# Optimization experiments

Hardware: AMD Instinct MI355X
Metric: run time of the kernel (lower is better)

## Reference

```python
import jax, jax.numpy as jnp
import numpy as np

EMBED_DIM = 1024
N_HEADS = 16
HEAD_DIM = EMBED_DIM // N_HEADS
B, N = 4, 2048


def setup_inputs() -> dict:
    key = jax.random.key(0)
    k1, k2, k3, k4, k5 = jax.random.split(key, 5)
    x = jax.random.normal(k1, (B, N, EMBED_DIM), dtype=jnp.float32)
    # Per-head kqv Linear weights stacked: torch Linear(embed_dim, 3*head_dim)
    # torch stores weight as [out, in]; we store transposed [in, out] per head.
    scale = 1.0 / np.sqrt(EMBED_DIM)
    W_kqv = jax.random.uniform(k2, (N_HEADS, EMBED_DIM, 3 * HEAD_DIM), dtype=jnp.float32, minval=-scale, maxval=scale)
    b_kqv = jax.random.uniform(k3, (N_HEADS, 3 * HEAD_DIM), dtype=jnp.float32, minval=-scale, maxval=scale)
    W_proj = jax.random.uniform(k4, (EMBED_DIM, EMBED_DIM), dtype=jnp.float32, minval=-scale, maxval=scale)
    b_proj = jax.random.uniform(k5, (EMBED_DIM,), dtype=jnp.float32, minval=-scale, maxval=scale)
    return {"x": x, "W_kqv": W_kqv, "b_kqv": b_kqv, "W_proj": W_proj, "b_proj": b_proj}


def reference(x, W_kqv, b_kqv, W_proj, b_proj):
    Bx, Nx, D = x.shape
    H = W_kqv.shape[0]
    hd = W_kqv.shape[2] // 3
    # All per-head kqv projections at once: [B, H, N, 3*hd]
    kqv = jnp.einsum('bnd,hde->bhne', x, W_kqv) + b_kqv[None, :, None, :]
    # chunk order in source is (k, q, v)
    k, q, v = jnp.split(kqv, 3, axis=-1)
    # scores scaled by sqrt(head_dim) (D1 in attention_scores is head dim)
    scores = jnp.einsum('bhqd,bhkd->bhqk', q, k) / jnp.sqrt(jnp.float32(hd))
    causal = jnp.tril(jnp.ones((Nx, Nx), dtype=bool))  # [N, N]
    scores = jnp.where(causal[None, None, :, :], scores, -jnp.inf)
    attn = jax.nn.softmax(scores, axis=-1)
    sa = jnp.einsum('bhqk,bhkd->bhqd', attn, v)  # [B, H, N, hd]
    # concat heads along feature dim (head order preserved)
    sa = sa.transpose(0, 2, 1, 3).reshape(Bx, Nx, H * hd)
    # output projection: torch Linear with weight [out, in] -> y = sa @ W^T + b;
    # here W_proj is stored as [in, out]
    return sa @ W_proj + b_proj
```

## Files before the change

### kernel.cpp

```cpp
#include <hip/hip_runtime.h>
#include <math.h>

#define EMBED   1024
#define NHEADS  16
#define HD      64
#define BATCH   4
#define SEQ     2048
#define MROWS   (BATCH*SEQ)
#define NKV     8388608ull

typedef short short8 __attribute__((ext_vector_type(8)));
typedef float floatx4 __attribute__((ext_vector_type(4)));

__device__ __forceinline__ unsigned short f2b(float f) {
    union { float f; unsigned u; } v; v.f = f;
    unsigned r = v.u + 0x7FFFu + ((v.u >> 16) & 1u);
    return (unsigned short)(r >> 16);
}
__device__ __forceinline__ unsigned short f2b_fast(float f) {
    union { float f; unsigned u; } v; v.f = f;
    return (unsigned short)((v.u + 0x8000u) >> 16);
}

#define GLDS16(gp, lp) __builtin_amdgcn_global_load_lds( \
    (const __attribute__((address_space(1))) unsigned int*)(gp), \
    (__attribute__((address_space(3))) unsigned int*)(lp), 16, 0, 0)

__global__ __launch_bounds__(256) void convert_x(
    const float* __restrict__ x, unsigned short* __restrict__ x16)
{
    size_t idx = ((size_t)blockIdx.x * 256 + threadIdx.x) * 8;
    float4 a = *(const float4*)(x + idx);
    float4 b = *(const float4*)(x + idx + 4);
    ushort4 u0, u1;
    u0.x = f2b(a.x); u0.y = f2b(a.y); u0.z = f2b(a.z); u0.w = f2b(a.w);
    u1.x = f2b(b.x); u1.y = f2b(b.y); u1.z = f2b(b.z); u1.w = f2b(b.w);
    *(ushort4*)(x16 + idx) = u0;
    *(ushort4*)(x16 + idx + 4) = u1;
}

__global__ __launch_bounds__(256) void prep_wkqv(
    const float* __restrict__ Wk, unsigned short* __restrict__ Wt)
{
    __shared__ float tile[32][33];
    const int h = blockIdx.z;
    const int k0 = blockIdx.x * 32, e0 = blockIdx.y * 32;
    const float* inh = Wk + (size_t)h * 1024 * 192;
    const int tx = threadIdx.x & 31, ty = threadIdx.x >> 5;
    #pragma unroll
    for (int i = 0; i < 4; i++)
        tile[ty + i * 8][tx] = inh[(size_t)(k0 + ty + i * 8) * 192 + e0 + tx];
    __syncthreads();
    #pragma unroll
    for (int i = 0; i < 4; i++) {
        int e = e0 + ty + i * 8;
        int cp = (e >> 6) * 1024 + h * 64 + (e & 63);
        Wt[(size_t)cp * 1024 + k0 + tx] = f2b(tile[tx][ty + i * 8]);
    }
}

__global__ __launch_bounds__(256) void transpose_w(
    const float* __restrict__ in, unsigned short* __restrict__ outp, int R, int C)
{
    __shared__ float tile[32][33];
    const int r0 = blockIdx.x * 32, c0 = blockIdx.y * 32;
    const int tx = threadIdx.x & 31, ty = threadIdx.x >> 5;
    #pragma unroll
    for (int i = 0; i < 4; i++)
        tile[ty + i * 8][tx] = in[(size_t)(r0 + ty + i * 8) * C + c0 + tx];
    __syncthreads();
    #pragma unroll
    for (int i = 0; i < 4; i++)
        outp[(size_t)(c0 + ty + i * 8) * R + r0 + tx] = f2b(tile[tx][ty + i * 8]);
}

__device__ __forceinline__ void mainloop_128x256(
    const unsigned short* __restrict__ Ag,
    const unsigned short* __restrict__ Bg,
    unsigned short* smem,
    int row0, int col0, floatx4 (&acc)[4][4])
{
    const int t = threadIdx.x;
    const int wave = t >> 6, lane = t & 63;
    const int lr = lane & 15, quad = lane >> 4;
    const int wr = wave >> 2, wc = wave & 3;
    const int swz8 = ((lane & 7) ^ ((lane >> 3) & 7)) * 8;
    const int c0 = (quad ^ (lr & 7)) * 8;
    const int c1 = ((4 + quad) ^ (lr & 7)) * 8;

    #pragma unroll
    for (int m = 0; m < 4; m++)
        #pragma unroll
        for (int n = 0; n < 4; n++) acc[m][n] = (floatx4){0.f, 0.f, 0.f, 0.f};

#define STG(G, R0, KC, L) do { \
    _Pragma("unroll") \
    for (int i_ = 0; i_ < 2; i_++) { \
        int rl_ = i_ * 64 + wave * 8 + (lane >> 3); \
        GLDS16((G) + (size_t)((R0) + rl_) * 1024 + (KC) + swz8, \
               (L) + rl_ * 64 + (lane & 7) * 8); \
    } } while (0)

    STG(Ag, row0,       0,  smem);
    STG(Bg, col0,       0,  smem + 8192);
    STG(Bg, col0 + 128, 0,  smem + 16384);
    STG(Bg, col0,       64, smem + 24576 + 8192);
    STG(Bg, col0 + 128, 64, smem + 24576 + 16384);
    asm volatile("s_waitcnt vmcnt(4)" ::: "memory");
    __builtin_amdgcn_s_barrier();

    #pragma unroll 2
    for (int j = 0; j < 16; ++j) {
        unsigned short* Ab = smem + (j & 1) * 24576;
        unsigned short* Bb = Ab + 8192;
        unsigned short* An = smem + ((j + 1) & 1) * 24576;
        const unsigned short* pA = Ab + (wr * 64 + lr) * 64;
        const unsigned short* pB = Bb + (wc * 64 + lr) * 64;

        short8 af0[4], af1[4], b0[4], b1[4];

        #pragma unroll
        for (int m = 0; m < 4; m++) af0[m] = *(const short8*)(pA + m * 1024 + c0);
        #pragma unroll
        for (int n = 0; n < 4; n++) b0[n] = *(const short8*)(pB + n * 1024 + c0);
        #pragma unroll
        for (int n = 0; n < 4; n++) b1[n] = *(const short8*)(pB + n * 1024 + c1);
        if (j < 15) STG(Ag, row0, (j + 1) * 64, An);
        __builtin_amdgcn_s_barrier();
        asm volatile("s_waitcnt lgkmcnt(0)" ::: "memory");
        __builtin_amdgcn_s_setprio(1);
        #pragma unroll
        for (int m = 0; m < 4; m++)
            #pragma unroll
            for (int n = 0; n < 4; n++)
                acc[m][n] = __builtin_amdgcn_mfma_f32_16x16x32_bf16(af0[m], b0[n], acc[m][n], 0, 0, 0);
        __builtin_amdgcn_s_setprio(0);
        __builtin_amdgcn_s_barrier();

        #pragma unroll
        for (int m = 0; m < 4; m++) af1[m] = *(const short8*)(pA + m * 1024 + c1);
        if (j < 14) {
            STG(Bg, col0,       (j + 2) * 64, Bb);
            STG(Bg, col0 + 128, (j + 2) * 64, Bb + 8192);
        }
        __builtin_amdgcn_s_barrier();
        asm volatile("s_waitcnt lgkmcnt(0)" ::: "memory");
        __builtin_amdgcn_s_setprio(1);
        #pragma unroll
        for (int m = 0; m < 4; m++)
            #pragma unroll
            for (int n = 0; n < 4; n++)
                acc[m][n] = __builtin_amdgcn_mfma_f32_16x16x32_bf16(af1[m], b1[n], acc[m][n], 0, 0, 0);
        __builtin_amdgcn_s_setprio(0);
        if (j < 14)       asm volatile("s_waitcnt vmcnt(4)" ::: "memory");
        else if (j == 14) asm volatile("s_waitcnt vmcnt(0)" ::: "memory");
        __builtin_amdgcn_s_barrier();
    }
#undef STG
}

__global__ __launch_bounds__(512, 2) void gemm_kqv(
    const unsigned short* __restrict__ A,
    const unsigned short* __restrict__ Bt,
    const float* __restrict__ bk,
    unsigned short* __restrict__ Kb16,
    unsigned short* __restrict__ Qb16,
    unsigned short* __restrict__ Vt16)
{
    __shared__ unsigned short smem[49152];

    const int mt = blockIdx.x;
    const int ct = blockIdx.y;
    const int row0 = mt * 128, col0 = ct * 256;

    floatx4 acc[4][4];
    mainloop_128x256(A, Bt, smem, row0, col0, acc);

    const int t = threadIdx.x;
    const int wave = t >> 6, lane = t & 63;
    const int lr = lane & 15, quad = lane >> 4;
    const int wr = wave >> 2, wc = wave & 3;

    unsigned short* W = smem + wave * 4096;
    const int sec = ct >> 2;
    const int h = ((ct & 3) << 2) + wc;
    const int bidx = row0 >> 11;
    const int rbase = (row0 & 2047) + wr * 64;

    float bias[4];
    #pragma unroll
    for (int n = 0; n < 4; n++) bias[n] = bk[h * 192 + sec * 64 + n * 16 + lr];

    if (sec < 2) {
        const float scl = (sec == 1) ? (0.125f * 1.44269504089f) : 1.0f;
        #pragma unroll
        for (int m = 0; m < 4; m++)
            #pragma unroll
            for (int n = 0; n < 4; n++) {
                int es = (n * 16 + lr) ^ (quad << 4);
                #pragma unroll
                for (int r = 0; r < 4; r++)
                    W[(m * 16 + quad * 4 + r) * 64 + es] = f2b((acc[m][n][r] + bias[n]) * scl);
            }
        __syncthreads();
        unsigned short* dst = ((sec == 0) ? Kb16 : Qb16)
                              + ((size_t)(bidx * 16 + h) * 2048 + rbase) * 64;
        const int rrow = lane >> 3, chunk = lane & 7;
        #pragma unroll
        for (int p = 0; p < 8; p++) {
            int row = p * 8 + rrow;
            int ch = chunk ^ (((row >> 2) & 3) << 1);
            *(float4*)(dst + (size_t)row * 64 + chunk * 8) =
                *(const float4*)(W + row * 64 + ch * 8);
        }
    } else {
        #pragma unroll
        for (int m = 0; m < 4; m++)
            #pragma unroll
            for (int n = 0; n < 4; n++) {
                int e = n * 16 + lr;
                ushort4 pk;
                pk.x = f2b(acc[m][n][0] + bias[n]);
                pk.y = f2b(acc[m][n][1] + bias[n]);
                pk.z = f2b(acc[m][n][2] + bias[n]);
                pk.w = f2b(acc[m][n][3] + bias[n]);
                int mp = m ^ (lr & 3);
                *(ushort4*)(W + e * 64 + mp * 16 + quad * 4) = pk;
            }
        __syncthreads();
        unsigned short* dstV = Vt16 + (size_t)(bidx * 16 + h) * 64 * 2048 + rbase;
        const int ev = lane >> 3, chunkR = lane & 7;
        #pragma unroll
        for (int p = 0; p < 8; p++) {
            int e = p * 8 + ev;
            int ch = chunkR ^ ((e & 3) << 1);
            *(float4*)(dstV + (size_t)e * 2048 + chunkR * 8) =
                *(const float4*)(W + e * 64 + ch * 8);
        }
    }
}

__global__ __launch_bounds__(256, 2) void attn_mfma(
    const unsigned short* __restrict__ Kb,
    const unsigned short* __restrict__ Qb,
    const unsigned short* __restrict__ Vt,
    unsigned short* __restrict__ sa)
{
    const int bx = blockIdx.x;
    const int bh = blockIdx.y;
    const int b = bh >> 4, h = bh & 15;
    const int wave = threadIdx.x >> 6;
    const int lane = threadIdx.x & 63;
    const int lr = lane & 15, quad = lane >> 4;
    const int qt_[2] = {bx, 15 - bx};

    __shared__ unsigned short Ks[64 * 64];
    __shared__ unsigned short Vs[64 * 64];
    __shared__ unsigned short Ps[4][2][16 * 72];

    const unsigned short* Kbh = Kb + (size_t)bh * 2048 * 64;
    const unsigned short* Vbh = Vt + (size_t)bh * 64 * 2048;
    const unsigned short* Qbh = Qb + (size_t)bh * 2048 * 64;

    short8 qf[2][2][2];
    #pragma unroll
    for (int tt = 0; tt < 2; tt++)
        #pragma unroll
        for (int s = 0; s < 2; s++) {
            const unsigned short* qp = Qbh +
                (size_t)(qt_[tt] * 128 + wave * 32 + s * 16 + lr) * 64 + quad * 8;
            qf[tt][s][0] = *(const short8*)(qp);
            qf[tt][s][1] = *(const short8*)(qp + 32);
        }

    floatx4 O[2][2][4];
    float ls[2][2][4];
    #pragma unroll
    for (int tt = 0; tt < 2; tt++)
        #pragma unroll
        for (int s = 0; s < 2; s++) {
            #pragma unroll
            for (int d = 0; d < 4; d++) O[tt][s][d] = (floatx4){0.f, 0.f, 0.f, 0.f};
            #pragma unroll
            for (int r = 0; r < 4; r++) ls[tt][s][r] = 0.f;
        }

    const int r_local = lane >> 3, cc = lane & 7;
    const int swz = cc ^ r_local;
    const int whalf = wave >> 1;

    const int ktmax = 2 * qt_[1] + 1;
    for (int kt = 0; kt <= ktmax; kt++) {
        const int k0 = kt * 64;
        __syncthreads();
        #pragma unroll
        for (int j = 0; j < 2; j++) {
            int R = wave * 16 + j * 8 + r_local;
            GLDS16(Kbh + (size_t)(k0 + R) * 64 + swz * 8, Ks + (wave * 16 + j * 8) * 64 + lane * 8);
            GLDS16(Vbh + (size_t)R * 2048 + k0 + swz * 8, Vs + (wave * 16 + j * 8) * 64 + lane * 8);
        }
        __syncthreads();

        #pragma unroll
        for (int tt = 0; tt < 2; tt++) {
            const int qt2 = qt_[tt];
            const int lim = 2 * qt2 + whalf;
            if (kt > lim) continue;

            floatx4 S[2][4];
            #pragma unroll
            for (int s = 0; s < 2; s++)
                #pragma unroll
                for (int a = 0; a < 4; a++) S[s][a] = (floatx4){0.f, 0.f, 0.f, 0.f};
            #pragma unroll
            for (int c = 0; c < 2; c++)
                #pragma unroll
                for (int a = 0; a < 4; a++) {
                    int R = a * 16 + lr;
                    short8 kf = *(const short8*)(Ks + R * 64 + (((c * 4 + quad) ^ (lr & 7)) * 8));
                    #pragma unroll
                    for (int s = 0; s < 2; s++)
                        S[s][a] = __builtin_amdgcn_mfma_f32_16x16x32_bf16(qf[tt][s][c], kf, S[s][a], 0, 0, 0);
                }

            if (kt == lim) {
                #pragma unroll
                for (int s = 0; s < 2; s++)
                    #pragma unroll
                    for (int a = 0; a < 4; a++) {
                        int col = k0 + a * 16 + lr;
                        #pragma unroll
                        for (int r = 0; r < 4; r++) {
                            int grow = qt2 * 128 + wave * 32 + s * 16 + quad * 4 + r;
                            if (col > grow) S[s][a][r] = -INFINITY;
                        }
                    }
            }

            #pragma unroll
            for (int s = 0; s < 2; s++)
                #pragma unroll
                for (int a = 0; a < 4; a++)
                    #pragma unroll
                    for (int r = 0; r < 4; r++) {
                        float p = __builtin_amdgcn_exp2f(S[s][a][r]);
                        ls[tt][s][r] += p;
                        Ps[wave][s][(quad * 4 + r) * 72 + a * 16 + lr] = f2b_fast(p);
                    }

            short8 pa[2][2];
            #pragma unroll
            for (int s = 0; s < 2; s++)
                #pragma unroll
                for (int c = 0; c < 2; c++)
                    pa[s][c] = *(const short8*)(Ps[wave][s] + lr * 72 + c * 32 + quad * 8);

            #pragma unroll
            for (int c = 0; c < 2; c++)
                #pragma unroll
                for (int d = 0; d < 4; d++) {
                    int R = d * 16 + lr;
                    short8 vf = *(const short8*)(Vs + R * 64 + (((c * 4 + quad) ^ (lr & 7)) * 8));
                    #pragma unroll
                    for (int s = 0; s < 2; s++)
                        O[tt][s][d] = __builtin_amdgcn_mfma_f32_16x16x32_bf16(pa[s][c], vf, O[tt][s][d], 0, 0, 0);
                }
        }
    }

    #pragma unroll
    for (int tt = 0; tt < 2; tt++)
        #pragma unroll
        for (int s = 0; s < 2; s++)
            #pragma unroll
            for (int r = 0; r < 4; r++) {
                float sm = ls[tt][s][r];
                sm += __shfl_xor(sm, 1);
                sm += __shfl_xor(sm, 2);
                sm += __shfl_xor(sm, 4);
                sm += __shfl_xor(sm, 8);
                float inv = 1.0f / sm;
                size_t base = ((size_t)(b * 2048 + qt_[tt] * 128 + wave * 32 + s * 16 + quad * 4 + r)) * 1024
                              + h * 64 + lr;
                #pragma unroll
                for (int d = 0; d < 4; d++)
                    sa[base + d * 16] = f2b(O[tt][s][d][r] * inv);
            }
}

__global__ __launch_bounds__(512, 2) void gemm_proj(
    const unsigned short* __restrict__ A,
    const unsigned short* __restrict__ Bt,
    const float* __restrict__ bp,
    float* __restrict__ out)
{
    __shared__ unsigned short smem[49152];

    const int mt = blockIdx.x;
    const int ct = blockIdx.y;
    const int row0 = mt * 128, col0 = ct * 256;

    floatx4 acc[4][4];
    mainloop_128x256(A, Bt, smem, row0, col0, acc);

    const int t = threadIdx.x;
    const int lane = t & 63, wave = t >> 6;
    const int lr = lane & 15, quad = lane >> 4;
    const int wr = wave >> 2, wc = wave & 3;

    float bias[4]; int cols[4];
    #pragma unroll
    for (int n = 0; n < 4; n++) {
        cols[n] = col0 + wc * 64 + n * 16 + lr;
        bias[n] = bp[cols[n]];
    }
    #pragma unroll
    for (int a = 0; a < 4; a++) {
        #pragma unroll
        for (int n = 0; n < 4; n++) {
            #pragma unroll
            for (int r = 0; r < 4; r++) {
                int m = row0 + wr * 64 + a * 16 + quad * 4 + r;
                out[(size_t)m * 1024 + cols[n]] = acc[a][n][r] + bias[n];
            }
        }
    }
}

extern "C" void kernel_launch(void* const* d_in, const int* in_sizes, int n_in,
                              void* d_out, int out_size, void* d_ws, size_t ws_size,
                              hipStream_t stream) {
    const float* x  = (const float*)d_in[0];
    const float* Wk = (const float*)d_in[1];
    const float* bk = (const float*)d_in[2];
    const float* Wp = (const float*)d_in[3];
    const float* bp = (const float*)d_in[4];
    float* out = (float*)d_out;

    unsigned short* Kb16 = (unsigned short*)d_ws;
    unsigned short* Qb16 = Kb16 + NKV;
    unsigned short* Vt16 = Qb16 + NKV;
    unsigned short* sa16 = Vt16 + NKV;
    unsigned short* x16  = sa16 + 8388608ull;
    unsigned short* Wt   = x16  + 8388608ull;
    unsigned short* Wpt  = Wt   + 3145728ull;

    convert_x<<<4096, 256, 0, stream>>>(x, x16);
    prep_wkqv<<<dim3(32, 6, 16), 256, 0, stream>>>(Wk, Wt);
    transpose_w<<<dim3(32, 32, 1), 256, 0, stream>>>(Wp, Wpt, 1024, 1024);
    gemm_kqv<<<dim3(64, 12), 512, 0, stream>>>(x16, Wt, bk, Kb16, Qb16, Vt16);
    attn_mfma<<<dim3(8, 64), 256, 0, stream>>>(Kb16, Qb16, Vt16, sa16);
    gemm_proj<<<dim3(64, 4), 512, 0, stream>>>(sa16, Wpt, bp, out);
}
```

Measured before the change: 245.4 us.

## Double-buffer K/V tiles in attention and swap grid dimension order

The attention kernel now keeps two LDS buffers for K and V. It issues the global-to-LDS loads for the next key tile before computing on the current one, and waits on vmcnt plus a barrier at the end of each iteration, replacing the two syncthreads per tile. The grid is also transposed so blockIdx.x walks batch-heads, which changes block scheduling order and L2 locality. The cost is doubled K/V LDS usage, which may affect occupancy at two blocks per CU.

Measured after the change: 234.3 us. 4.5% less time.

```diff
diff --git a/kernel.cpp b/kernel.cpp
--- a/kernel.cpp
+++ b/kernel.cpp
@@ -246,16 +246,16 @@
     const unsigned short* __restrict__ Vt,
     unsigned short* __restrict__ sa)
 {
-    const int bx = blockIdx.x;
-    const int bh = blockIdx.y;
+    const int bh = blockIdx.x;
+    const int bx = blockIdx.y;
     const int b = bh >> 4, h = bh & 15;
     const int wave = threadIdx.x >> 6;
     const int lane = threadIdx.x & 63;
     const int lr = lane & 15, quad = lane >> 4;
     const int qt_[2] = {bx, 15 - bx};
 
-    __shared__ unsigned short Ks[64 * 64];
-    __shared__ unsigned short Vs[64 * 64];
+    __shared__ unsigned short Ks[2][64 * 64];
+    __shared__ unsigned short Vs[2][64 * 64];
     __shared__ unsigned short Ps[4][2][16 * 72];
 
     const unsigned short* Kbh = Kb + (size_t)bh * 2048 * 64;
@@ -289,17 +289,33 @@
     const int swz = cc ^ r_local;
     const int whalf = wave >> 1;
 
+#define STAGE_KV(KT, BSEL) do { \
+    const int k0_ = (KT) * 64; \
+    _Pragma("unroll") \
+    for (int j_ = 0; j_ < 2; j_++) { \
+        int R_ = wave * 16 + j_ * 8 + r_local; \
+        GLDS16(Kbh + (size_t)(k0_ + R_) * 64 + swz * 8, \
+               &Ks[BSEL][0] + (wave * 16 + j_ * 8) * 64 + lane * 8); \
+        GLDS16(Vbh + (size_t)R_ * 2048 + k0_ + swz * 8, \
+               &Vs[BSEL][0] + (wave * 16 + j_ * 8) * 64 + lane * 8); \
+    } } while (0)
+
     const int ktmax = 2 * qt_[1] + 1;
+
+    STAGE_KV(0, 0);
+    asm volatile("s_waitcnt vmcnt(0)" ::: "memory");
+    __builtin_amdgcn_s_barrier();
+
     for (int kt = 0; kt <= ktmax; kt++) {
+        const int buf = kt & 1;
+        const unsigned short* Ksb = &Ks[buf][0];
+        const unsigned short* Vsb = &Vs[buf][0];
         const int k0 = kt * 64;
-        __syncthreads();
-        #pragma unroll
-        for (int j = 0; j < 2; j++) {
-            int R = wave * 16 + j * 8 + r_local;
-            GLDS16(Kbh + (size_t)(k0 + R) * 64 + swz * 8, Ks + (wave * 16 + j * 8) * 64 + lane * 8);
-            GLDS16(Vbh + (size_t)R * 2048 + k0 + swz * 8, Vs + (wave * 16 + j * 8) * 64 + lane * 8);
-        }
-        __syncthreads();
+
+        if (kt < ktmax) {
+            if (buf) STAGE_KV(kt + 1, 0);
+            else     STAGE_KV(kt + 1, 1);
+        }
 
         #pragma unroll
         for (int tt = 0; tt < 2; tt++) {
@@ -317,7 +333,7 @@
                 #pragma unroll
                 for (int a = 0; a < 4; a++) {
                     int R = a * 16 + lr;
-                    short8 kf = *(const short8*)(Ks + R * 64 + (((c * 4 + quad) ^ (lr & 7)) * 8));
+                    short8 kf = *(const short8*)(Ksb + R * 64 + (((c * 4 + quad) ^ (lr & 7)) * 8));
                     #pragma unroll
                     for (int s = 0; s < 2; s++)
                         S[s][a] = __builtin_amdgcn_mfma_f32_16x16x32_bf16(qf[tt][s][c], kf, S[s][a], 0, 0, 0);
@@ -360,13 +376,17 @@
                 #pragma unroll
                 for (int d = 0; d < 4; d++) {
                     int R = d * 16 + lr;
-                    short8 vf = *(const short8*)(Vs + R * 64 + (((c * 4 + quad) ^ (lr & 7)) * 8));
+                    short8 vf = *(const short8*)(Vsb + R * 64 + (((c * 4 + quad) ^ (lr & 7)) * 8));
                     #pragma unroll
                     for (int s = 0; s < 2; s++)
                         O[tt][s][d] = __builtin_amdgcn_mfma_f32_16x16x32_bf16(pa[s][c], vf, O[tt][s][d], 0, 0, 0);
                 }
         }
-    }
+
+        asm volatile("s_waitcnt vmcnt(0)" ::: "memory");
+        __builtin_amdgcn_s_barrier();
+    }
+#undef STAGE_KV
 
     #pragma unroll
     for (int tt = 0; tt < 2; tt++)
@@ -449,6 +469,6 @@
     prep_wkqv<<<dim3(32, 6, 16), 256, 0, stream>>>(Wk, Wt);
     transpose_w<<<dim3(32, 32, 1), 256, 0, stream>>>(Wp, Wpt, 1024, 1024);
     gemm_kqv<<<dim3(64, 12), 512, 0, stream>>>(x16, Wt, bk, Kb16, Qb16, Vt16);
-    attn_mfma<<<dim3(8, 64), 256, 0, stream>>>(Kb16, Qb16, Vt16, sa16);
+    attn_mfma<<<dim3(64, 8), 256, 0, stream>>>(Kb16, Qb16, Vt16, sa16);
     gemm_proj<<<dim3(64, 4), 512, 0, stream>>>(sa16, Wpt, bp, out);
 }
```
